# Kernel optimization log

Hardware: AMD Instinct MI355X
Metric: run time of the kernel (lower is better)

## Reference

```python
import jax, jax.numpy as jnp
import numpy as np

T, B, D, H, N = 2048, 8, 1024, 16, 32


def setup_inputs() -> dict:
    key = jax.random.key(0)
    ks = jax.random.split(key, 6)
    s = 1.0 / np.sqrt(D)  # xavier-ish scale
    return {
        "x": jax.random.normal(ks[0], (T, B, D), jnp.float32),
        "S0": jnp.zeros((B, H, N, N), jnp.float32),
        "W_in": jax.random.normal(ks[1], (D, D), jnp.float32) * s,
        "W_k": jax.random.normal(ks[2], (H * N, D), jnp.float32) * s,
        "W_v": jax.random.normal(ks[3], (H * N, D), jnp.float32) * s,
        "W_q": jax.random.normal(ks[4], (H * N, D), jnp.float32) * s,
        "W_beta": jax.random.normal(ks[5], (H * N, D), jnp.float32) * s,
        "b_beta": jnp.full((H, N), 2.0, jnp.float32),  # init_beta_bias=2.0
    }


def reference(x, S0, W_in, W_k, W_v, W_q, W_beta, b_beta):
    # x: [T,B,D] -> in_proj (expansion=1.0 so d_inner == D)
    Tn, Bn, Dn = x.shape
    Hh, Nn = b_beta.shape
    xp = jnp.einsum('tbd,ed->tbe', x, W_in)  # [T,B,D]
    # projections to [T,B,H,N]
    k = jnp.einsum('tbd,fd->tbf', xp, W_k).reshape(Tn, Bn, Hh, Nn)
    v = jnp.einsum('tbd,fd->tbf', xp, W_v).reshape(Tn, Bn, Hh, Nn)
    q = jnp.einsum('tbd,fd->tbf', xp, W_q).reshape(Tn, Bn, Hh, Nn)
    beta = jax.nn.sigmoid(
        jnp.einsum('tbd,fd->tbf', xp, W_beta).reshape(Tn, Bn, Hh, Nn) + b_beta)

    def step(S, inputs):
        # S: [B,H,N,N]; each input: [B,H,N]
        k_t, v_t, q_t, beta_t = inputs
        k_norm = k_t / (jnp.linalg.norm(k_t, axis=-1, keepdims=True) + 1e-6)
        retrieved = jnp.einsum('bhij,bhj->bhi', S, k_norm)
        delta = v_t - retrieved
        outer = delta[..., :, None] * k_norm[..., None, :]  # [B,H,N,N]
        S_new = jnp.tanh(beta_t[..., None] * S + outer)
        Sq = jnp.einsum('bhij,bhj->bhi', S_new, q_t)
        out_t = Sq * (Sq * jax.nn.sigmoid(Sq))  # Sq * silu(Sq)
        return S_new, out_t

    S_final, outs = jax.lax.scan(step, S0, (k, v, q, beta))
    output = outs.reshape(Tn, Bn, Hh * Nn)  # [T,B,H*N]
    return output, S_final
```

## Files before the change

### kernel.cpp

```cpp
#include <hip/hip_runtime.h>
#include <hip/hip_bf16.h>
#include <stdint.h>

#define TT 2048
#define BB 8
#define DD 1024
#define FF 2048
#define HN 512
#define KB_CNT 32
#define ROWB 128
#define MSTRIDE 4096
#define PF 8

typedef float f32x4 __attribute__((ext_vector_type(4)));
typedef float f32x2 __attribute__((ext_vector_type(2)));
typedef _Float16 h8_t __attribute__((ext_vector_type(8)));

#define CC   2.88539008f
#define SQC  1.69864360f

__device__ __forceinline__ float fexp2(float x){ return __builtin_amdgcn_exp2f(x); }
__device__ __forceinline__ float frcp(float x){ return __builtin_amdgcn_rcpf(x); }
__device__ __forceinline__ float fsqrt_(float x){ return __builtin_amdgcn_sqrtf(x); }
__device__ __forceinline__ float fast_sigmoid(float x){
    return frcp(1.0f + fexp2(-1.44269504f * x));
}

template<int CTRL>
__device__ __forceinline__ float dppadd(float v){
    int x = __builtin_amdgcn_update_dpp(0, __float_as_int(v), CTRL, 0xf, 0xf, true);
    return v + __int_as_float(x);
}
__device__ __forceinline__ float reduce16(float v){
    v = dppadd<0xB1>(v);
    v = dppadd<0x4E>(v);
    v = dppadd<0x141>(v);
    v = dppadd<0x140>(v);
    return v;
}

__device__ __forceinline__ void split8(const float* f, int4& hi, int4& lo){
    union { _Float16 h[8]; int4 i; } a, c;
    #pragma unroll
    for (int u = 0; u < 8; ++u) {
        _Float16 h = (_Float16)f[u];
        a.h[u] = h;
        c.h[u] = (_Float16)(f[u] - (float)h);
    }
    hi = a.i; lo = c.i;
}

__global__ __launch_bounds__(256)
void gemm_f32c(const float* __restrict__ s0, const float* __restrict__ s1,
               const float* __restrict__ s2, const float* __restrict__ s3,
               const float* __restrict__ B, float* __restrict__ C)
{
    __shared__ __align__(16) float As[16][68];
    __shared__ __align__(16) float Bs[16][72];
    const int tid = threadIdx.x;
    const int tx = tid & 15, ty = tid >> 4;
    const int n0 = blockIdx.x * 64, m0 = blockIdx.y * 64;
    float acc[4][4] = {};

    const int arow = tid >> 2, ac4 = (tid & 3) << 2;
    const int f = m0 + arow;
    const float* asrc = ((f < 512) ? s0 : (f < 1024) ? s1 : (f < 1536) ? s2 : s3)
                        + (size_t)(f & 511) * DD + ac4;
    const int bk = tid >> 4, bc = tid & 15;

    for (int k0 = 0; k0 < DD; k0 += 16) {
        float4 av = *(const float4*)(asrc + k0);
        As[ac4+0][arow] = av.x; As[ac4+1][arow] = av.y;
        As[ac4+2][arow] = av.z; As[ac4+3][arow] = av.w;
        float4 bv = *(const float4*)&B[(size_t)(k0 + bk) * DD + n0 + bc * 4];
        int p = bc + (bc >> 3);
        *(float4*)&Bs[bk][p << 2] = bv;
        __syncthreads();
        #pragma unroll
        for (int kk = 0; kk < 16; ++kk) {
            float a[4], b[4];
            *(float4*)&a[0] = *(const float4*)&As[kk][ty * 4];
            int p2 = tx + (tx >> 3);
            *(float4*)&b[0] = *(const float4*)&Bs[kk][p2 << 2];
            #pragma unroll
            for (int i = 0; i < 4; ++i)
                #pragma unroll
                for (int j = 0; j < 4; ++j)
                    acc[i][j] = __builtin_fmaf(a[i], b[j], acc[i][j]);
        }
        __syncthreads();
    }
    #pragma unroll
    for (int ii = 0; ii < 4; ++ii) {
        float4 v;
        v.x = acc[ii][0]; v.y = acc[ii][1]; v.z = acc[ii][2]; v.w = acc[ii][3];
        *(float4*)&C[(size_t)(m0 + ty * 4 + ii) * DD + n0 + tx * 4] = v;
    }
}

__global__ __launch_bounds__(256)
void wconv(const float* __restrict__ W, char* __restrict__ out)
{
    int gid = blockIdx.x * 256 + threadIdx.x;
    int n  = gid >> 6;
    int kh = gid & 63;
    const float* src = W + (size_t)n * DD + kh * 16;
    float f[16];
    *(float4*)&f[0]  = *(const float4*)(src + 0);
    *(float4*)&f[4]  = *(const float4*)(src + 4);
    *(float4*)&f[8]  = *(const float4*)(src + 8);
    *(float4*)&f[12] = *(const float4*)(src + 12);
    int4 hi0, hi1, lo0, lo1;
    split8(&f[0], hi0, lo0);
    split8(&f[8], hi1, lo1);
    int kb = kh >> 1, c0 = (kh & 1) * 2, rs = n & 7;
    char* dst = out + (size_t)n * MSTRIDE + kb * ROWB;
    *(int4*)(dst + (((c0+0) ^ rs) * 16)) = hi0;
    *(int4*)(dst + (((c0+1) ^ rs) * 16)) = hi1;
    *(int4*)(dst + (((c0+4) ^ rs) * 16)) = lo0;
    *(int4*)(dst + (((c0+5) ^ rs) * 16)) = lo1;
}

__global__ __launch_bounds__(512, 1)
void gemm_mfma8(const char* __restrict__ Axp, const char* __restrict__ Wsp,
                float* __restrict__ C, const float* __restrict__ bias)
{
    extern __shared__ char ldsb[];
    const int tid  = threadIdx.x;
    const int wave = tid >> 6, lane = tid & 63;
    const int wm = wave >> 2, wn = wave & 3;
    const int nt = blockIdx.x & 7, mt = blockIdx.x >> 3;
    const int m0 = mt * 256, n0 = nt * 256;

    f32x4 acc[8][4] = {};

    const char* aT = Axp + (size_t)(m0 + wave * 32 + (lane >> 3)) * MSTRIDE + (lane & 7) * 16;
    const char* bT = Wsp + (size_t)(n0 + wave * 32 + (lane >> 3)) * MSTRIDE + (lane & 7) * 16;
    const int ldst = (wave * 32) * 128;

    const int fl = lane & 15, fh = lane >> 4;
    const int shi = (fh ^ (fl & 7)) * 16;
    const int slo = ((fh + 4) ^ (fl & 7)) * 16;

    {
        char* L = ldsb;
        #pragma unroll
        for (int g = 0; g < 4; ++g)
            __builtin_amdgcn_global_load_lds(
                (const __attribute__((address_space(1))) uint32_t*)(aT + (size_t)g * 8 * MSTRIDE),
                (__attribute__((address_space(3))) uint32_t*)(L + ldst + g * 1024),
                16, 0, 0);
        #pragma unroll
        for (int g = 0; g < 4; ++g)
            __builtin_amdgcn_global_load_lds(
                (const __attribute__((address_space(1))) uint32_t*)(bT + (size_t)g * 8 * MSTRIDE),
                (__attribute__((address_space(3))) uint32_t*)(L + 32768 + ldst + g * 1024),
                16, 0, 0);
    }

    union u8 { int4 i; h8_t h; };
    u8 Ah[4], Al[4], Bh[4], Bl[4];

    for (int t = 0; t < KB_CNT; ++t) {
        char* Lc = ldsb + (t & 1) * 65536;
        char* Ln = ldsb + ((t + 1) & 1) * 65536;
        const bool stg = (t + 1 < KB_CNT);
        const char* aN = aT + ROWB;
        const char* bN = bT + ROWB;

        asm volatile("s_waitcnt vmcnt(0)" ::: "memory");
        __builtin_amdgcn_s_barrier();
        asm volatile("" ::: "memory");

        if (stg) {
            #pragma unroll
            for (int g = 0; g < 4; ++g)
                __builtin_amdgcn_global_load_lds(
                    (const __attribute__((address_space(1))) uint32_t*)(aN + (size_t)g * 8 * MSTRIDE),
                    (__attribute__((address_space(3))) uint32_t*)(Ln + ldst + g * 1024),
                    16, 0, 0);
            #pragma unroll
            for (int g = 0; g < 4; ++g)
                __builtin_amdgcn_global_load_lds(
                    (const __attribute__((address_space(1))) uint32_t*)(bN + (size_t)g * 8 * MSTRIDE),
                    (__attribute__((address_space(3))) uint32_t*)(Ln + 32768 + ldst + g * 1024),
                    16, 0, 0);
        }

        #pragma unroll
        for (int f = 0; f < 4; ++f) {
            const char* base = Lc + (wm * 128 + f * 16 + fl) * 128;
            Ah[f].i = *(const int4*)(base + shi);
            Al[f].i = *(const int4*)(base + slo);
        }
        #pragma unroll
        for (int f = 0; f < 4; ++f) {
            const char* base = Lc + 32768 + (wn * 64 + f * 16 + fl) * 128;
            Bh[f].i = *(const int4*)(base + shi);
            Bl[f].i = *(const int4*)(base + slo);
        }
        __builtin_amdgcn_s_setprio(1);
        #pragma unroll
        for (int i = 0; i < 4; ++i)
            #pragma unroll
            for (int j = 0; j < 4; ++j)
                acc[i][j] = __builtin_amdgcn_mfma_f32_16x16x32_f16(Ah[i].h, Bh[j].h, acc[i][j], 0, 0, 0);
        #pragma unroll
        for (int i = 0; i < 4; ++i)
            #pragma unroll
            for (int j = 0; j < 4; ++j)
                acc[i][j] = __builtin_amdgcn_mfma_f32_16x16x32_f16(Ah[i].h, Bl[j].h, acc[i][j], 0, 0, 0);
        #pragma unroll
        for (int i = 0; i < 4; ++i)
            #pragma unroll
            for (int j = 0; j < 4; ++j)
                acc[i][j] = __builtin_amdgcn_mfma_f32_16x16x32_f16(Al[i].h, Bh[j].h, acc[i][j], 0, 0, 0);
        __builtin_amdgcn_s_setprio(0);

        #pragma unroll
        for (int f = 0; f < 4; ++f) {
            const char* base = Lc + (wm * 128 + (f + 4) * 16 + fl) * 128;
            Ah[f].i = *(const int4*)(base + shi);
            Al[f].i = *(const int4*)(base + slo);
        }
        __builtin_amdgcn_s_setprio(1);
        #pragma unroll
        for (int i = 0; i < 4; ++i)
            #pragma unroll
            for (int j = 0; j < 4; ++j)
                acc[i + 4][j] = __builtin_amdgcn_mfma_f32_16x16x32_f16(Ah[i].h, Bh[j].h, acc[i + 4][j], 0, 0, 0);
        #pragma unroll
        for (int i = 0; i < 4; ++i)
            #pragma unroll
            for (int j = 0; j < 4; ++j)
                acc[i + 4][j] = __builtin_amdgcn_mfma_f32_16x16x32_f16(Ah[i].h, Bl[j].h, acc[i + 4][j], 0, 0, 0);
        #pragma unroll
        for (int i = 0; i < 4; ++i)
            #pragma unroll
            for (int j = 0; j < 4; ++j)
                acc[i + 4][j] = __builtin_amdgcn_mfma_f32_16x16x32_f16(Al[i].h, Bh[j].h, acc[i + 4][j], 0, 0, 0);
        __builtin_amdgcn_s_setprio(0);

        aT += ROWB; bT += ROWB;
    }

    const int blk = nt >> 1;
    if (blk == 0) {
        #pragma unroll
        for (int fm = 0; fm < 8; ++fm)
            #pragma unroll
            for (int hg = 0; hg < 2; ++hg)
                #pragma unroll
                for (int reg = 0; reg < 4; ++reg) {
                    float a = acc[fm][hg*2][reg], c = acc[fm][hg*2+1][reg];
                    float p = __builtin_fmaf(a, a, c * c);
                    p = reduce16(p);
                    float rn = SQC * frcp(fsqrt_(p) + 1e-6f);
                    acc[fm][hg*2][reg]   = a * rn;
                    acc[fm][hg*2+1][reg] = c * rn;
                }
    }

    const int sub = (blk == 0) ? 0 : (blk == 2) ? 1 : (blk == 1) ? 2 : 3;
    #pragma unroll
    for (int fm = 0; fm < 8; ++fm) {
        int rbase = m0 + wm * 128 + fm * 16 + fh * 4;
        #pragma unroll
        for (int fn = 0; fn < 4; ++fn) {
            int col = n0 + wn * 64 + fn * 16 + fl;
            int hh  = (col >> 5) & 15;
            int idx = col & 31;
            float bb = (blk == 3) ? bias[col - 3 * HN] : 0.0f;
            #pragma unroll
            for (int reg = 0; reg < 4; ++reg) {
                float v = acc[fm][fn][reg];
                if (blk == 1) v = SQC * v;
                else if (blk == 3) v = CC * fast_sigmoid(v + bb);
                *(float*)((char*)C + (size_t)(rbase + reg) * 8192
                          + hh * 512 + sub * 128 + idx * 4) = v;
            }
        }
    }
}

template<bool PRE>
__global__ __launch_bounds__(256)
void gemm_mfma(const float* __restrict__ A, const char* __restrict__ Axp,
               const char* __restrict__ Wsp,
               float* __restrict__ C, const float* __restrict__ bias)
{
    __shared__ char lds[32768];
    char* Asb = lds;
    char* Bsb = lds + 16384;

    const int tid  = threadIdx.x;
    const int wave = tid >> 6, lane = tid & 63;
    const int wm = wave >> 1, wn = wave & 1;
    const int nt = blockIdx.x & 15, mt = blockIdx.x >> 4;
    const int m0 = mt * 128, n0 = nt * 128;

    f32x4 acc[4][4] = {};

    const int ar = tid >> 1, akh = tid & 1, ars = ar & 7, ac0 = akh * 2;
    const float* asrc = A + (size_t)(m0 + ar) * DD + akh * 16;
    char* awr = Asb + ar * ROWB;

    const char* bsrc_base = Wsp + (size_t)n0 * MSTRIDE;
    const char* asrc_base = Axp + (size_t)m0 * MSTRIDE;

    const int fl = lane & 15, fh = lane >> 4;
    const int shi = (fh ^ (fl & 7)) * 16;
    const int slo = ((fh + 4) ^ (fl & 7)) * 16;
    const int frow = fl * ROWB;

    for (int ks = 0; ks < KB_CNT; ++ks) {
        #pragma unroll
        for (int gg = 0; gg < 4; ++gg) {
            int g = wave * 4 + gg;
            const char* src = bsrc_base + (size_t)(g * 8 + (lane >> 3)) * MSTRIDE
                              + ks * ROWB + (lane & 7) * 16;
            __builtin_amdgcn_global_load_lds(
                (const __attribute__((address_space(1))) uint32_t*)src,
                (__attribute__((address_space(3))) uint32_t*)(Bsb + g * 1024),
                16, 0, 0);
        }
        if (PRE) {
            #pragma unroll
            for (int gg = 0; gg < 4; ++gg) {
                int g = wave * 4 + gg;
                const char* src = asrc_base + (size_t)(g * 8 + (lane >> 3)) * MSTRIDE
                                  + ks * ROWB + (lane & 7) * 16;
                __builtin_amdgcn_global_load_lds(
                    (const __attribute__((address_space(1))) uint32_t*)src,
                    (__attribute__((address_space(3))) uint32_t*)(Asb + g * 1024),
                    16, 0, 0);
            }
        } else {
            const float* ap = asrc + ks * 32;
            float f[16];
            *(float4*)&f[0]  = *(const float4*)(ap + 0);
            *(float4*)&f[4]  = *(const float4*)(ap + 4);
            *(float4*)&f[8]  = *(const float4*)(ap + 8);
            *(float4*)&f[12] = *(const float4*)(ap + 12);
            int4 hi0, hi1, lo0, lo1;
            split8(&f[0], hi0, lo0);
            split8(&f[8], hi1, lo1);
            *(int4*)(awr + (((ac0+0) ^ ars) * 16)) = hi0;
            *(int4*)(awr + (((ac0+1) ^ ars) * 16)) = hi1;
            *(int4*)(awr + (((ac0+4) ^ ars) * 16)) = lo0;
            *(int4*)(awr + (((ac0+5) ^ ars) * 16)) = lo1;
        }
        __syncthreads();

        union { int4 i; h8_t h; } ah[4], al[4], bh[4], bl[4];
        #pragma unroll
        for (int fm = 0; fm < 4; ++fm) {
            const char* base = Asb + (wm * 64 + fm * 16) * ROWB + frow;
            ah[fm].i = *(const int4*)(base + shi);
            al[fm].i = *(const int4*)(base + slo);
        }
        #pragma unroll
        for (int fn = 0; fn < 4; ++fn) {
            const char* base = Bsb + (wn * 64 + fn * 16) * ROWB + frow;
            bh[fn].i = *(const int4*)(base + shi);
            bl[fn].i = *(const int4*)(base + slo);
        }
        #pragma unroll
        for (int fm = 0; fm < 4; ++fm)
            #pragma unroll
            for (int fn = 0; fn < 4; ++fn) {
                acc[fm][fn] = __builtin_amdgcn_mfma_f32_16x16x32_f16(ah[fm].h, bh[fn].h, acc[fm][fn], 0, 0, 0);
                acc[fm][fn] = __builtin_amdgcn_mfma_f32_16x16x32_f16(ah[fm].h, bl[fn].h, acc[fm][fn], 0, 0, 0);
                acc[fm][fn] = __builtin_amdgcn_mfma_f32_16x16x32_f16(al[fm].h, bh[fn].h, acc[fm][fn], 0, 0, 0);
            }
        __syncthreads();
    }

    const int blk = nt >> 2;
    if (blk == 0) {
        #pragma unroll
        for (int fm = 0; fm < 4; ++fm)
            #pragma unroll
            for (int hg = 0; hg < 2; ++hg)
                #pragma unroll
                for (int reg = 0; reg < 4; ++reg) {
                    float a = acc[fm][hg*2][reg], c = acc[fm][hg*2+1][reg];
                    float p = __builtin_fmaf(a, a, c * c);
                    p = reduce16(p);
                    float rn = SQC * frcp(fsqrt_(p) + 1e-6f);
                    acc[fm][hg*2][reg]   = a * rn;
                    acc[fm][hg*2+1][reg] = c * rn;
                }
    }

    const int sub = (blk == 0) ? 0 : (blk == 2) ? 1 : (blk == 1) ? 2 : 3;
    #pragma unroll
    for (int fm = 0; fm < 4; ++fm) {
        int rbase = m0 + wm * 64 + fm * 16 + fh * 4;
        #pragma unroll
        for (int fn = 0; fn < 4; ++fn) {
            int col = n0 + wn * 64 + fn * 16 + fl;
            int hh  = (col >> 5) & 15;
            int idx = col & 31;
            float bb = (blk == 3) ? bias[col - 3 * HN] : 0.0f;
            #pragma unroll
            for (int reg = 0; reg < 4; ++reg) {
                float v = acc[fm][fn][reg];
                if (blk == 1) v = SQC * v;
                else if (blk == 3) v = CC * fast_sigmoid(v + bb);
                *(float*)((char*)C + (size_t)(rbase + reg) * 8192
                          + hh * 512 + sub * 128 + idx * 4) = v;
            }
        }
    }
}

__global__ __launch_bounds__(256)
void recur(const float* __restrict__ proj, const float* __restrict__ S0,
           float* __restrict__ out, float* __restrict__ Sfin)
{
    const int tid = threadIdx.x;
    const int bx  = blockIdx.x;
    const int bh  = bx >> 1;
    const int b   = bh >> 4, h = bh & 15;
    const int i   = ((bx & 1) << 4) + (tid >> 4);
    const int jl  = tid & 15;

    f32x2 S;
    {
        const float* s0p = S0 + (size_t)bh * 1024 + i * 32 + 2 * jl;
        S[0] = s0p[0]; S[1] = s0p[1];
    }

    const char* pkq = (const char*)proj + (size_t)b * 8192 + h * 512 + jl * 8;
    const char* pvb = (const char*)proj + (size_t)b * 8192 + h * 512 + 256 + i * 4;
    const size_t rstep = (size_t)BB * 8192;

    f32x2 K2[PF], Q2[PF];
    float V[PF], Bt[PF];

    #pragma unroll
    for (int p = 0; p < PF; ++p) {
        asm volatile("global_load_dwordx2 %0, %1, off"            : "=v"(K2[p]) : "v"(pkq));
        asm volatile("global_load_dwordx2 %0, %1, off offset:128" : "=v"(Q2[p]) : "v"(pkq));
        asm volatile("global_load_dword %0, %1, off"              : "=v"(V[p])  : "v"(pvb));
        asm volatile("global_load_dword %0, %1, off offset:128"   : "=v"(Bt[p]) : "v"(pvb));
        pkq += rstep; pvb += rstep;
    }

    asm volatile("s_waitcnt vmcnt(28)" : "+v"(V[0]), "+v"(Bt[0]));
    float cv = V[0];
    f32x2 bS = Bt[0] * S;

    float* pout = out + (size_t)b * HN + h * 32 + i;

    for (int t0 = 0; t0 < TT; t0 += PF) {
        float osave[PF];
        #pragma unroll
        for (int p = 0; p < PF; ++p) {
            const int pn = (p + 1) & (PF - 1);
            asm volatile("s_waitcnt vmcnt(24)"
                : "+v"(K2[p]), "+v"(Q2[p]), "+v"(V[pn]), "+v"(Bt[pn]));

            f32x2 k2 = K2[p];
            float rr = __builtin_fmaf(S[1], k2[1], S[0] * k2[0]);
            rr = reduce16(rr);
            float d = cv - rr;
            f32x2 a = d * k2 + bS;
            f32x2 e; e[0] = fexp2(a[0]); e[1] = fexp2(a[1]);
            f32x2 e1 = e + 1.0f;
            f32x2 r; r[0] = frcp(e1[0]); r[1] = frcp(e1[1]);
            S = -2.0f * r + 1.0f;

            f32x2 q2 = Q2[p];
            osave[p] = __builtin_fmaf(S[1], q2[1], S[0] * q2[0]);

            cv = V[pn];
            bS = Bt[pn] * S;

            asm volatile("global_load_dwordx2 %0, %1, off"            : "=v"(K2[p]) : "v"(pkq));
            asm volatile("global_load_dwordx2 %0, %1, off offset:128" : "=v"(Q2[p]) : "v"(pkq));
            asm volatile("global_load_dword %0, %1, off"              : "=v"(V[p])  : "v"(pvb));
            asm volatile("global_load_dword %0, %1, off offset:128"   : "=v"(Bt[p]) : "v"(pvb));
            pkq += rstep; pvb += rstep;
        }
        #pragma unroll
        for (int p = 0; p < PF; ++p) osave[p] = reduce16(osave[p]);
        if (jl == 0) {
            #pragma unroll
            for (int p = 0; p < PF; ++p) {
                float sq = osave[p];
                float sg = fast_sigmoid(sq);
                pout[(size_t)p * (BB * HN)] = sq * sq * sg;
            }
        }
        pout += (size_t)PF * (BB * HN);
    }

    {
        float* sf = Sfin + (size_t)bh * 1024 + i * 32 + 2 * jl;
        sf[0] = S[0]; sf[1] = S[1];
    }
}

extern "C" void kernel_launch(void* const* d_in, const int* in_sizes, int n_in,
                              void* d_out, int out_size, void* d_ws, size_t ws_size,
                              hipStream_t stream) {
    const float* x      = (const float*)d_in[0];
    const float* S0     = (const float*)d_in[1];
    const float* W_in   = (const float*)d_in[2];
    const float* W_k    = (const float*)d_in[3];
    const float* W_v    = (const float*)d_in[4];
    const float* W_q    = (const float*)d_in[5];
    const float* W_beta = (const float*)d_in[6];
    const float* b_beta = (const float*)d_in[7];

    float* ws   = (float*)d_ws;
    float* out_ = (float*)d_out;
    float* Sfin = out_ + (size_t)TT * BB * HN;

    const size_t NEED_PRE = (size_t)(33554432 + 16777216 + 2*2097152) * 4;
    const bool pre = (ws_size >= NEED_PRE);

    if (pre) {
        float* proj   = ws;
        char*  xsplit = (char*)(ws + 33554432);
        float* Weff   = ws + 33554432 + 16777216;
        char*  wsplit = (char*)(Weff + 2097152);

        hipError_t aerr = hipFuncSetAttribute(
            reinterpret_cast<const void*>(&gemm_mfma8),
            hipFuncAttributeMaxDynamicSharedMemorySize, 131072);

        gemm_f32c<<<dim3(16, 32), dim3(256), 0, stream>>>(W_k, W_v, W_q, W_beta, W_in, Weff);
        wconv<<<dim3(512), dim3(256), 0, stream>>>(Weff, wsplit);
        wconv<<<dim3(4096), dim3(256), 0, stream>>>(x, xsplit);
        if (aerr == hipSuccess) {
            gemm_mfma8<<<dim3(512), dim3(512), 131072, stream>>>(xsplit, wsplit, proj, b_beta);
        } else {
            gemm_mfma<true><<<dim3(2048), dim3(256), 0, stream>>>(x, xsplit, wsplit, proj, b_beta);
        }
        recur<<<dim3(256), dim3(256), 0, stream>>>(proj, S0, out_, Sfin);
    } else {
        float* proj   = ws;
        float* Weff   = ws + 33554432;
        char*  wsplit = (char*)(Weff + 2097152);

        gemm_f32c<<<dim3(16, 32), dim3(256), 0, stream>>>(W_k, W_v, W_q, W_beta, W_in, Weff);
        wconv<<<dim3(512), dim3(256), 0, stream>>>(Weff, wsplit);
        gemm_mfma<false><<<dim3(2048), dim3(256), 0, stream>>>(x, nullptr, wsplit, proj, b_beta);
        recur<<<dim3(256), dim3(256), 0, stream>>>(proj, S0, out_, Sfin);
    }
}
```

Baseline: 525.0 us.

## Interleave k/q and v/beta in projection layout and deepen recurrence prefetch

The GEMM epilogues now write the projection buffer with k and q interleaved per pair and v and beta interleaved per element. This lets the recurrence kernel fetch each timestep with one dwordx4 and one dwordx2 load instead of four separate loads. The prefetch depth goes from 8 to 16 timesteps, and the output reduction and store now happen every step instead of being batched per 8. This cuts load-instruction count and lengthens latency hiding on the serial recurrence, at the cost of more registers and a per-step output reduction that sits on the critical path.

```diff
diff --git a/kernel.cpp b/kernel.cpp
--- a/kernel.cpp
+++ b/kernel.cpp
@@ -10,7 +10,6 @@
 #define KB_CNT 32
 #define ROWB 128
 #define MSTRIDE 4096
-#define PF 8
 
 typedef float f32x4 __attribute__((ext_vector_type(4)));
 typedef float f32x2 __attribute__((ext_vector_type(2)));
@@ -121,6 +120,14 @@
     *(int4*)(dst + (((c0+5) ^ rs) * 16)) = lo1;
 }
 
+#define EPI_STORE(Cb, rbase, reg, hh, idx, blk, v, bb) { \
+    char* rowp = (char*)(Cb) + (size_t)((rbase) + (reg)) * 8192 + (hh) * 512; \
+    if ((blk) == 0)      *(float*)(rowp + ((idx) >> 1) * 16 + ((idx) & 1) * 4) = (v); \
+    else if ((blk) == 2) *(float*)(rowp + ((idx) >> 1) * 16 + 8 + ((idx) & 1) * 4) = (v); \
+    else if ((blk) == 1) *(float*)(rowp + 256 + (idx) * 8) = SQC * (v); \
+    else                 *(float*)(rowp + 256 + (idx) * 8 + 4) = CC * fast_sigmoid((v) + (bb)); \
+}
+
 __global__ __launch_bounds__(512, 1)
 void gemm_mfma8(const char* __restrict__ Axp, const char* __restrict__ Wsp,
                 float* __restrict__ C, const float* __restrict__ bias)
@@ -261,7 +268,6 @@
                 }
     }
 
-    const int sub = (blk == 0) ? 0 : (blk == 2) ? 1 : (blk == 1) ? 2 : 3;
     #pragma unroll
     for (int fm = 0; fm < 8; ++fm) {
         int rbase = m0 + wm * 128 + fm * 16 + fh * 4;
@@ -274,10 +280,7 @@
             #pragma unroll
             for (int reg = 0; reg < 4; ++reg) {
                 float v = acc[fm][fn][reg];
-                if (blk == 1) v = SQC * v;
-                else if (blk == 3) v = CC * fast_sigmoid(v + bb);
-                *(float*)((char*)C + (size_t)(rbase + reg) * 8192
-                          + hh * 512 + sub * 128 + idx * 4) = v;
+                EPI_STORE(C, rbase, reg, hh, idx, blk, v, bb);
             }
         }
     }
@@ -393,7 +396,6 @@
                 }
     }
 
-    const int sub = (blk == 0) ? 0 : (blk == 2) ? 1 : (blk == 1) ? 2 : 3;
     #pragma unroll
     for (int fm = 0; fm < 4; ++fm) {
         int rbase = m0 + wm * 64 + fm * 16 + fh * 4;
@@ -406,16 +408,13 @@
             #pragma unroll
             for (int reg = 0; reg < 4; ++reg) {
                 float v = acc[fm][fn][reg];
-                if (blk == 1) v = SQC * v;
-                else if (blk == 3) v = CC * fast_sigmoid(v + bb);
-                *(float*)((char*)C + (size_t)(rbase + reg) * 8192
-                          + hh * 512 + sub * 128 + idx * 4) = v;
+                EPI_STORE(C, rbase, reg, hh, idx, blk, v, bb);
             }
         }
     }
 }
 
-__global__ __launch_bounds__(256)
+__global__ __launch_bounds__(256, 1)
 void recur(const float* __restrict__ proj, const float* __restrict__ S0,
            float* __restrict__ out, float* __restrict__ Sfin)
 {
@@ -432,75 +431,65 @@
         S[0] = s0p[0]; S[1] = s0p[1];
     }
 
-    const char* pkq = (const char*)proj + (size_t)b * 8192 + h * 512 + jl * 8;
-    const char* pvb = (const char*)proj + (size_t)b * 8192 + h * 512 + 256 + i * 4;
+    const char* pkq = (const char*)proj + (size_t)b * 8192 + h * 512 + jl * 16;
+    const char* pvb = (const char*)proj + (size_t)b * 8192 + h * 512 + 256 + i * 8;
     const size_t rstep = (size_t)BB * 8192;
 
-    f32x2 K2[PF], Q2[PF];
-    float V[PF], Bt[PF];
-
-    #pragma unroll
-    for (int p = 0; p < PF; ++p) {
-        asm volatile("global_load_dwordx2 %0, %1, off"            : "=v"(K2[p]) : "v"(pkq));
-        asm volatile("global_load_dwordx2 %0, %1, off offset:128" : "=v"(Q2[p]) : "v"(pkq));
-        asm volatile("global_load_dword %0, %1, off"              : "=v"(V[p])  : "v"(pvb));
-        asm volatile("global_load_dword %0, %1, off offset:128"   : "=v"(Bt[p]) : "v"(pvb));
-        pkq += rstep; pvb += rstep;
-    }
-
-    asm volatile("s_waitcnt vmcnt(28)" : "+v"(V[0]), "+v"(Bt[0]));
-    float cv = V[0];
-    f32x2 bS = Bt[0] * S;
+#define RDECL(p) f32x4 KQ##p; f32x2 VB##p;
+    RDECL(0) RDECL(1) RDECL(2) RDECL(3) RDECL(4) RDECL(5) RDECL(6) RDECL(7)
+    RDECL(8) RDECL(9) RDECL(10) RDECL(11) RDECL(12) RDECL(13) RDECL(14) RDECL(15)
+
+#define RISSUE(p) \
+    asm volatile("global_load_dwordx4 %0, %1, off" : "=v"(KQ##p) : "v"(pkq)); \
+    asm volatile("global_load_dwordx2 %0, %1, off" : "=v"(VB##p) : "v"(pvb)); \
+    pkq += rstep; pvb += rstep;
+
+    RISSUE(0) RISSUE(1) RISSUE(2) RISSUE(3) RISSUE(4) RISSUE(5) RISSUE(6) RISSUE(7)
+    RISSUE(8) RISSUE(9) RISSUE(10) RISSUE(11) RISSUE(12) RISSUE(13) RISSUE(14) RISSUE(15)
+
+    asm volatile("s_waitcnt vmcnt(30)" : "+v"(VB0));
+    float cv = VB0[0];
+    f32x2 bS = VB0[1] * S;
 
     float* pout = out + (size_t)b * HN + h * 32 + i;
 
-    for (int t0 = 0; t0 < TT; t0 += PF) {
-        float osave[PF];
-        #pragma unroll
-        for (int p = 0; p < PF; ++p) {
-            const int pn = (p + 1) & (PF - 1);
-            asm volatile("s_waitcnt vmcnt(24)"
-                : "+v"(K2[p]), "+v"(Q2[p]), "+v"(V[pn]), "+v"(Bt[pn]));
-
-            f32x2 k2 = K2[p];
-            float rr = __builtin_fmaf(S[1], k2[1], S[0] * k2[0]);
-            rr = reduce16(rr);
-            float d = cv - rr;
-            f32x2 a = d * k2 + bS;
-            f32x2 e; e[0] = fexp2(a[0]); e[1] = fexp2(a[1]);
-            f32x2 e1 = e + 1.0f;
-            f32x2 r; r[0] = frcp(e1[0]); r[1] = frcp(e1[1]);
-            S = -2.0f * r + 1.0f;
-
-            f32x2 q2 = Q2[p];
-            osave[p] = __builtin_fmaf(S[1], q2[1], S[0] * q2[0]);
-
-            cv = V[pn];
-            bS = Bt[pn] * S;
-
-            asm volatile("global_load_dwordx2 %0, %1, off"            : "=v"(K2[p]) : "v"(pkq));
-            asm volatile("global_load_dwordx2 %0, %1, off offset:128" : "=v"(Q2[p]) : "v"(pkq));
-            asm volatile("global_load_dword %0, %1, off"              : "=v"(V[p])  : "v"(pvb));
-            asm volatile("global_load_dword %0, %1, off offset:128"   : "=v"(Bt[p]) : "v"(pvb));
-            pkq += rstep; pvb += rstep;
-        }
-        #pragma unroll
-        for (int p = 0; p < PF; ++p) osave[p] = reduce16(osave[p]);
-        if (jl == 0) {
-            #pragma unroll
-            for (int p = 0; p < PF; ++p) {
-                float sq = osave[p];
-                float sg = fast_sigmoid(sq);
-                pout[(size_t)p * (BB * HN)] = sq * sq * sg;
-            }
-        }
-        pout += (size_t)PF * (BB * HN);
+#define RSTEP(p, pn) { \
+    asm volatile("s_waitcnt vmcnt(28)" : "+v"(KQ##p), "+v"(VB##pn)); \
+    f32x4 kq = KQ##p; \
+    float rr = __builtin_fmaf(S[1], kq[1], S[0] * kq[0]); \
+    rr = reduce16(rr); \
+    float d = cv - rr; \
+    f32x2 k2; k2[0] = kq[0]; k2[1] = kq[1]; \
+    f32x2 a = d * k2 + bS; \
+    f32x2 e; e[0] = fexp2(a[0]); e[1] = fexp2(a[1]); \
+    f32x2 e1 = e + 1.0f; \
+    f32x2 r; r[0] = frcp(e1[0]); r[1] = frcp(e1[1]); \
+    S = -2.0f * r + 1.0f; \
+    float sq = __builtin_fmaf(S[1], kq[3], S[0] * kq[2]); \
+    sq = reduce16(sq); \
+    if (jl == 0) { float sg = fast_sigmoid(sq); *pout = sq * sq * sg; } \
+    pout += BB * HN; \
+    cv = VB##pn[0]; \
+    bS = VB##pn[1] * S; \
+    asm volatile("global_load_dwordx4 %0, %1, off" : "=v"(KQ##p) : "v"(pkq)); \
+    asm volatile("global_load_dwordx2 %0, %1, off" : "=v"(VB##p) : "v"(pvb)); \
+    pkq += rstep; pvb += rstep; \
+}
+
+    for (int t0 = 0; t0 < TT; t0 += 16) {
+        RSTEP(0,1)  RSTEP(1,2)   RSTEP(2,3)   RSTEP(3,4)
+        RSTEP(4,5)  RSTEP(5,6)   RSTEP(6,7)   RSTEP(7,8)
+        RSTEP(8,9)  RSTEP(9,10)  RSTEP(10,11) RSTEP(11,12)
+        RSTEP(12,13) RSTEP(13,14) RSTEP(14,15) RSTEP(15,0)
     }
 
     {
         float* sf = Sfin + (size_t)bh * 1024 + i * 32 + 2 * jl;
         sf[0] = S[0]; sf[1] = S[1];
     }
+#undef RSTEP
+#undef RISSUE
+#undef RDECL
 }
 
 extern "C" void kernel_launch(void* const* d_in, const int* in_sizes, int n_in,
```

Result: slower. 592.0 us (+12.8%).
